# Optimization experiments

Hardware: AMD Instinct MI355X
Metric: run time of the kernel (lower is better)

## Reference

```python
import jax, jax.numpy as jnp
import numpy as np

# dims per module source / chosen globals
B, LB = 4, 28            # new frames, buffered frames; M = B+LB = L = 32
DK, DV = 256, 32         # Dk=256 hardcoded; Dv = 4*len_of_lookup+4 with len_of_lookup=7
HS, WS = 64, 64          # H//8, W//8 with H=W=512
LMAX = 32                # memory cap L
TRAIN_SZ = 1000          # log base train_sz
ALPHA = 0.5              # blend coefficient (original inits 0, which zeroes the branch)
# log(L*h*w + h*w, train_sz) / sqrt(Dk)
SCALE = float(np.log(LMAX * HS * WS + HS * WS) / np.log(TRAIN_SZ) / np.sqrt(DK))


def _xavier(key, fan_in, fan_out):
    lim = np.sqrt(6.0 / (fan_in + fan_out))
    return jax.random.uniform(key, (fan_in, fan_out), jnp.float32, -lim, lim)


def setup_inputs() -> dict:
    key = jax.random.key(0)
    ks = jax.random.split(key, 7)
    return {
        "fc": jax.random.normal(ks[0], (B, DK, HS, WS), jnp.float32),
        "fm": jax.random.normal(ks[1], (B, DV, HS, WS), jnp.float32),
        "key_buffer": jax.random.normal(ks[2], (LB, DK, HS, WS), jnp.float32),
        "value_buffer": jax.random.normal(ks[3], (LB, DV, HS, WS), jnp.float32),
        "Q": _xavier(ks[4], DK, DK),
        "K": _xavier(ks[5], DK, DK),
        "V": _xavier(ks[6], DV, DV),
    }


def reference(fc, fm, key_buffer, value_buffer, Q, K, V):
    # matmul = einsum('ijkl,jm->imkl'): per-pixel channel mixing
    q = jnp.einsum('bdhw,de->behw', fc, Q)                      # [B,Dk,h,w]
    k = jnp.concatenate([jnp.einsum('bdhw,de->behw', fc, K), key_buffer], axis=0)    # [M,Dk,h,w]
    v = jnp.concatenate([jnp.einsum('bdhw,de->behw', fm, V), value_buffer], axis=0)  # [M,Dv,h,w]
    # current_batch (=1) < L, so no slicing of k/v on this step
    scores = SCALE * jnp.einsum('bdhw,mdhw->bmhw', q, k)        # [B,M,h,w]
    attn = jax.nn.softmax(scores, axis=-1)                      # NOTE: softmax over width axis, as in source (dim=-1)
    ctx = jnp.einsum('bmhw,mdhw->bdhw', attn, v)                # [B,Dv,h,w]
    return fm + ALPHA * ctx
```

## Files before the change

### kernel.cpp

```cpp
#include <hip/hip_runtime.h>
#include <hip/hip_bf16.h>
#include <cmath>

#define NB 4
#define NM 32
#define DKc 256
#define DVc 32
#define NP 4096

using bf16x8 = __attribute__((ext_vector_type(8))) short;
using f32x4  = __attribute__((ext_vector_type(4))) float;

__device__ __forceinline__ unsigned short f2bf(float f) {
    union { float f; unsigned u; } x; x.f = f;
    unsigned r = 0x7FFFu + ((x.u >> 16) & 1u);
    return (unsigned short)((x.u + r) >> 16);
}
__device__ __forceinline__ float bflo(unsigned u) { union { unsigned u; float f; } x; x.u = u << 16; return x.f; }
__device__ __forceinline__ float bfhi(unsigned u) { union { unsigned u; float f; } x; x.u = u & 0xffff0000u; return x.f; }
__device__ __forceinline__ float bf2f(unsigned short s) { union { unsigned u; float f; } x; x.u = ((unsigned)s) << 16; return x.f; }

__global__ __launch_bounds__(256) void k_transpose_bf16(
    const float* __restrict__ src, unsigned short* __restrict__ dst,
    int R, int C, long batchStride) {
    __shared__ float tile[64][65];
    int b = blockIdx.z;
    const float* s = src + (long)b * batchStride;
    unsigned short* d = dst + (long)b * batchStride;
    int r0 = blockIdx.y * 64, c0 = blockIdx.x * 64;
    int t = threadIdx.x;
    #pragma unroll
    for (int j = 0; j < 16; ++j) {
        int i = t + 256 * j;
        int r = i >> 6, c = i & 63;
        tile[r][c] = s[(long)(r0 + r) * C + c0 + c];
    }
    __syncthreads();
    #pragma unroll
    for (int j = 0; j < 8; ++j) {
        int i = t + 256 * j;
        int row = i >> 5;
        int pr = i & 31;
        float f0 = tile[2 * pr][row];
        float f1 = tile[2 * pr + 1][row];
        unsigned pack = (unsigned)f2bf(f0) | ((unsigned)f2bf(f1) << 16);
        reinterpret_cast<unsigned*>(d)[(((long)(c0 + row) * R + r0) >> 1) + pr] = pack;
    }
}

__global__ __launch_bounds__(256) void k_vproj(
    const float* __restrict__ fm, const float* __restrict__ V, float* __restrict__ vproj) {
    __shared__ float Vl[32][32];
    __shared__ float fml[32][256];
    int b = blockIdx.y, p0 = blockIdx.x * 256, t = threadIdx.x;
    #pragma unroll
    for (int j = 0; j < 4; ++j) { int i = t + 256 * j; Vl[i >> 5][i & 31] = V[i]; }
    for (int j = 0; j < 32; ++j) {
        int i = t + 256 * j;
        int dd = i >> 8, c = i & 255;
        fml[dd][c] = fm[((long)b * DVc + dd) * NP + p0 + c];
    }
    __syncthreads();
    float acc[32];
    #pragma unroll
    for (int e = 0; e < 32; ++e) acc[e] = 0.f;
    for (int dd = 0; dd < 32; ++dd) {
        float fv = fml[dd][t];
        #pragma unroll
        for (int e = 0; e < 32; ++e) acc[e] += fv * Vl[dd][e];
    }
    #pragma unroll
    for (int e = 0; e < 32; ++e) vproj[((long)b * DVc + e) * NP + p0 + t] = acc[e];
}

__global__ __launch_bounds__(256) void k_proj_gemm(
    const unsigned short* __restrict__ WTq, const unsigned short* __restrict__ WTk,
    const unsigned short* __restrict__ fcT,
    unsigned short* __restrict__ qT, float* __restrict__ kproj) {
    int t = threadIdx.x;
    int wave = t >> 6, lane = t & 63;
    int b = blockIdx.z & 3, mat = blockIdx.z >> 2;
    int e0 = blockIdx.y * 64 + wave * 16;
    int p0 = blockIdx.x * 64;
    int ln = lane & 15, quad = lane >> 4;
    const unsigned short* WT = mat ? WTk : WTq;
    const unsigned short* aptr = WT + (long)(e0 + ln) * DKc + quad * 8;
    const unsigned short* bbase = fcT + ((long)b * NP + p0 + ln) * DKc + quad * 8;
    f32x4 acc[4] = {};
    for (int kk = 0; kk < DKc; kk += 32) {
        bf16x8 a = *reinterpret_cast<const bf16x8*>(aptr + kk);
        #pragma unroll
        for (int j = 0; j < 4; ++j) {
            bf16x8 bb = *reinterpret_cast<const bf16x8*>(bbase + (long)j * 16 * DKc + kk);
            acc[j] = __builtin_amdgcn_mfma_f32_16x16x32_bf16(a, bb, acc[j], 0, 0, 0);
        }
    }
    int eb = e0 + quad * 4;
    if (mat == 0) {
        #pragma unroll
        for (int j = 0; j < 4; ++j)
            #pragma unroll
            for (int r = 0; r < 4; ++r) {
                int e = eb + r, p = p0 + j * 16 + ln;
                qT[((long)b * NP + p) * DKc + e] = f2bf(acc[j][r]);
            }
    } else {
        #pragma unroll
        for (int j = 0; j < 4; ++j)
            #pragma unroll
            for (int r = 0; r < 4; ++r) {
                int e = eb + r, p = p0 + j * 16 + ln;
                kproj[((long)b * DKc + e) * NP + p] = acc[j][r];
            }
    }
}

__global__ __launch_bounds__(512) void k_scores(
    const unsigned short* __restrict__ qT, const float* __restrict__ kproj,
    const float* __restrict__ kbuf, float* __restrict__ scores, float scale) {
    __shared__ float red[16][4][4][32];
    int t = threadIdx.x;
    int g = t >> 5, p = t & 31;
    int p0 = blockIdx.x * 32;
    int mg = blockIdx.y;
    float qreg[4][16];
    #pragma unroll
    for (int b = 0; b < 4; ++b) {
        const uint4* qp4 = reinterpret_cast<const uint4*>(qT + ((long)b * NP + p0 + p) * DKc + g * 16);
        uint4 u0 = qp4[0], u1 = qp4[1];
        unsigned w[8] = {u0.x, u0.y, u0.z, u0.w, u1.x, u1.y, u1.z, u1.w};
        #pragma unroll
        for (int j = 0; j < 8; ++j) { qreg[b][2 * j] = bflo(w[j]); qreg[b][2 * j + 1] = bfhi(w[j]); }
    }
    for (int c = 0; c < 4; ++c) {
        float acc[4][4];
        #pragma unroll
        for (int mi = 0; mi < 4; ++mi)
            #pragma unroll
            for (int b = 0; b < 4; ++b) acc[mi][b] = 0.f;
        #pragma unroll
        for (int mi = 0; mi < 4; ++mi) {
            int m = mg * 16 + c * 4 + mi;
            const float* kp = (m < 4 ? kproj + (long)m * DKc * NP : kbuf + (long)(m - 4) * DKc * NP)
                              + (long)(g * 16) * NP + p0 + p;
            #pragma unroll
            for (int j = 0; j < 16; ++j) {
                float kv = kp[(long)j * NP];
                acc[mi][0] += qreg[0][j] * kv;
                acc[mi][1] += qreg[1][j] * kv;
                acc[mi][2] += qreg[2][j] * kv;
                acc[mi][3] += qreg[3][j] * kv;
            }
        }
        #pragma unroll
        for (int mi = 0; mi < 4; ++mi)
            #pragma unroll
            for (int b = 0; b < 4; ++b) red[g][mi][b][p] = acc[mi][b];
        __syncthreads();
        {
            int mi = t >> 7, b = (t >> 5) & 3, pp = t & 31;
            float s = 0.f;
            #pragma unroll
            for (int gg = 0; gg < 16; ++gg) s += red[gg][mi][b][pp];
            int m = mg * 16 + c * 4 + mi;
            scores[((long)b * NM + m) * NP + p0 + pp] = scale * s;
        }
        __syncthreads();
    }
}

__global__ __launch_bounds__(256) void k_out(
    const float* __restrict__ scores, const float* __restrict__ vproj,
    const float* __restrict__ vbuf, const float* __restrict__ fm,
    float* __restrict__ out) {
    __shared__ unsigned short attn[128][130];
    int t = threadIdx.x;
    int p0 = blockIdx.x * 128;
    int dq = blockIdx.y;
    {
        int b = t >> 6, mrow = (t >> 1) & 31, hs = t & 1;
        const f32x4* s4 = reinterpret_cast<const f32x4*>(scores + ((long)b * NM + mrow) * NP + p0 + hs * 64);
        f32x4 v[16];
        #pragma unroll
        for (int j = 0; j < 16; ++j) v[j] = s4[j];
        float mx = v[0][0];
        #pragma unroll
        for (int j = 0; j < 16; ++j)
            #pragma unroll
            for (int k = 0; k < 4; ++k) mx = fmaxf(mx, v[j][k]);
        float sum = 0.f;
        #pragma unroll
        for (int j = 0; j < 16; ++j)
            #pragma unroll
            for (int k = 0; k < 4; ++k) { float e = __expf(v[j][k] - mx); v[j][k] = e; sum += e; }
        float inv = 1.f / sum;
        unsigned short* arow = &attn[(b << 5) | mrow][hs * 64];
        #pragma unroll
        for (int j = 0; j < 16; ++j)
            #pragma unroll
            for (int k = 0; k < 4; ++k) arow[j * 4 + k] = f2bf(v[j][k] * inv);
    }
    __syncthreads();
    int p = t & 127, grp = t >> 7;
    int b0 = grp * 2, b1 = grp * 2 + 1;
    float acc0[8], acc1[8];
    #pragma unroll
    for (int d = 0; d < 8; ++d) { acc0[d] = 0.f; acc1[d] = 0.f; }
    for (int m = 0; m < 32; ++m) {
        float a0 = bf2f(attn[b0 * 32 + m][p]);
        float a1 = bf2f(attn[b1 * 32 + m][p]);
        const float* vbp = (m < 4 ? vproj + (long)m * DVc * NP : vbuf + (long)(m - 4) * DVc * NP)
                           + (long)(dq * 8) * NP + p0 + p;
        #pragma unroll
        for (int d = 0; d < 8; ++d) {
            float vv = vbp[(long)d * NP];
            acc0[d] += a0 * vv;
            acc1[d] += a1 * vv;
        }
    }
    #pragma unroll
    for (int d = 0; d < 8; ++d) {
        long i0 = ((long)b0 * DVc + dq * 8 + d) * NP + p0 + p;
        out[i0] = fm[i0] + 0.5f * acc0[d];
        long i1 = ((long)b1 * DVc + dq * 8 + d) * NP + p0 + p;
        out[i1] = fm[i1] + 0.5f * acc1[d];
    }
}

extern "C" void kernel_launch(void* const* d_in, const int* in_sizes, int n_in,
                              void* d_out, int out_size, void* d_ws, size_t ws_size,
                              hipStream_t stream) {
    const float* fc = (const float*)d_in[0];
    const float* fm = (const float*)d_in[1];
    const float* kb = (const float*)d_in[2];
    const float* vb = (const float*)d_in[3];
    const float* Q  = (const float*)d_in[4];
    const float* K  = (const float*)d_in[5];
    const float* V  = (const float*)d_in[6];
    float* out = (float*)d_out;
    char* ws = (char*)d_ws;
    unsigned short* fcT   = (unsigned short*)(ws);
    unsigned short* WTq   = (unsigned short*)(ws + 8388608);
    unsigned short* WTk   = (unsigned short*)(ws + 8519680);
    unsigned short* qT    = (unsigned short*)(ws + 8650752);
    float*          kproj = (float*)(ws + 17039360);
    float*          vproj = (float*)(ws + 33816576);
    float*          scores= (float*)(ws + 35913728);
    float scale = (float)(log(135168.0) / log(1000.0) / 16.0);

    hipLaunchKernelGGL(k_transpose_bf16, dim3(64, 4, 4), dim3(256), 0, stream,
                       fc, fcT, 256, 4096, (long)256 * 4096);
    hipLaunchKernelGGL(k_transpose_bf16, dim3(4, 4, 1), dim3(256), 0, stream,
                       Q, WTq, 256, 256, (long)0);
    hipLaunchKernelGGL(k_transpose_bf16, dim3(4, 4, 1), dim3(256), 0, stream,
                       K, WTk, 256, 256, (long)0);
    hipLaunchKernelGGL(k_vproj, dim3(16, 4), dim3(256), 0, stream, fm, V, vproj);
    hipLaunchKernelGGL(k_proj_gemm, dim3(64, 4, 8), dim3(256), 0, stream,
                       WTq, WTk, fcT, qT, kproj);
    hipLaunchKernelGGL(k_scores, dim3(128, 2), dim3(512), 0, stream,
                       qT, kproj, kb, scores, scale);
    hipLaunchKernelGGL(k_out, dim3(32, 4), dim3(256), 0, stream,
                       scores, vproj, vb, fm, out);
}
```

Before: 267.5 us.

## Fuse scores, softmax and output into one kernel; merge prep kernels; widen GEMM tiles

```diff
diff --git a/kernel.cpp b/kernel.cpp
--- a/kernel.cpp
+++ b/kernel.cpp
@@ -16,214 +16,227 @@
     unsigned r = 0x7FFFu + ((x.u >> 16) & 1u);
     return (unsigned short)((x.u + r) >> 16);
 }
-__device__ __forceinline__ float bflo(unsigned u) { union { unsigned u; float f; } x; x.u = u << 16; return x.f; }
-__device__ __forceinline__ float bfhi(unsigned u) { union { unsigned u; float f; } x; x.u = u & 0xffff0000u; return x.f; }
 __device__ __forceinline__ float bf2f(unsigned short s) { union { unsigned u; float f; } x; x.u = ((unsigned)s) << 16; return x.f; }
 
-__global__ __launch_bounds__(256) void k_transpose_bf16(
-    const float* __restrict__ src, unsigned short* __restrict__ dst,
-    int R, int C, long batchStride) {
-    __shared__ float tile[64][65];
-    int b = blockIdx.z;
-    const float* s = src + (long)b * batchStride;
-    unsigned short* d = dst + (long)b * batchStride;
-    int r0 = blockIdx.y * 64, c0 = blockIdx.x * 64;
+__global__ __launch_bounds__(256) void k_prep(
+    const float* __restrict__ fc, unsigned short* __restrict__ fcT,
+    const float* __restrict__ Q, unsigned short* __restrict__ WTq,
+    const float* __restrict__ K, unsigned short* __restrict__ WTk,
+    const float* __restrict__ fm, const float* __restrict__ V, float* __restrict__ vproj) {
+    int x = blockIdx.x;
     int t = threadIdx.x;
-    #pragma unroll
-    for (int j = 0; j < 16; ++j) {
-        int i = t + 256 * j;
-        int r = i >> 6, c = i & 63;
-        tile[r][c] = s[(long)(r0 + r) * C + c0 + c];
-    }
-    __syncthreads();
-    #pragma unroll
-    for (int j = 0; j < 8; ++j) {
-        int i = t + 256 * j;
-        int row = i >> 5;
-        int pr = i & 31;
-        float f0 = tile[2 * pr][row];
-        float f1 = tile[2 * pr + 1][row];
-        unsigned pack = (unsigned)f2bf(f0) | ((unsigned)f2bf(f1) << 16);
-        reinterpret_cast<unsigned*>(d)[(((long)(c0 + row) * R + r0) >> 1) + pr] = pack;
-    }
-}
-
-__global__ __launch_bounds__(256) void k_vproj(
-    const float* __restrict__ fm, const float* __restrict__ V, float* __restrict__ vproj) {
-    __shared__ float Vl[32][32];
-    __shared__ float fml[32][256];
-    int b = blockIdx.y, p0 = blockIdx.x * 256, t = threadIdx.x;
-    #pragma unroll
-    for (int j = 0; j < 4; ++j) { int i = t + 256 * j; Vl[i >> 5][i & 31] = V[i]; }
-    for (int j = 0; j < 32; ++j) {
-        int i = t + 256 * j;
-        int dd = i >> 8, c = i & 255;
-        fml[dd][c] = fm[((long)b * DVc + dd) * NP + p0 + c];
-    }
-    __syncthreads();
-    float acc[32];
-    #pragma unroll
-    for (int e = 0; e < 32; ++e) acc[e] = 0.f;
-    for (int dd = 0; dd < 32; ++dd) {
-        float fv = fml[dd][t];
-        #pragma unroll
-        for (int e = 0; e < 32; ++e) acc[e] += fv * Vl[dd][e];
-    }
-    #pragma unroll
-    for (int e = 0; e < 32; ++e) vproj[((long)b * DVc + e) * NP + p0 + t] = acc[e];
-}
-
-__global__ __launch_bounds__(256) void k_proj_gemm(
+    if (x < 1056) {
+        __shared__ float tile[64][65];
+        const float* s; unsigned short* d; int R, C, r0, c0;
+        if (x < 1024) {
+            int bb = x >> 8, rest = x & 255;
+            R = 256; C = 4096;
+            r0 = (rest >> 6) * 64; c0 = (rest & 63) * 64;
+            s = fc + (long)bb * 256 * 4096; d = fcT + (long)bb * 256 * 4096;
+        } else {
+            int i = x - 1024;
+            int mat = i >> 4, idx = i & 15;
+            R = 256; C = 256;
+            r0 = (idx >> 2) * 64; c0 = (idx & 3) * 64;
+            s = mat ? K : Q; d = mat ? WTk : WTq;
+        }
+        #pragma unroll
+        for (int j = 0; j < 16; ++j) {
+            int i = t + 256 * j;
+            int r = i >> 6, c = i & 63;
+            tile[r][c] = s[(long)(r0 + r) * C + c0 + c];
+        }
+        __syncthreads();
+        #pragma unroll
+        for (int j = 0; j < 8; ++j) {
+            int i = t + 256 * j;
+            int row = i >> 5;
+            int pr = i & 31;
+            float f0 = tile[2 * pr][row];
+            float f1 = tile[2 * pr + 1][row];
+            unsigned pack = (unsigned)f2bf(f0) | ((unsigned)f2bf(f1) << 16);
+            reinterpret_cast<unsigned*>(d)[(((long)(c0 + row) * R + r0) >> 1) + pr] = pack;
+        }
+    } else {
+        __shared__ float Vl[32][32];
+        __shared__ float fml[32][256];
+        int i = x - 1056;
+        int b = i >> 4, p0 = (i & 15) * 256;
+        #pragma unroll
+        for (int j = 0; j < 4; ++j) { int ii = t + 256 * j; Vl[ii >> 5][ii & 31] = V[ii]; }
+        for (int j = 0; j < 32; ++j) {
+            int ii = t + 256 * j;
+            int dd = ii >> 8, c = ii & 255;
+            fml[dd][c] = fm[((long)b * DVc + dd) * NP + p0 + c];
+        }
+        __syncthreads();
+        float acc[32];
+        #pragma unroll
+        for (int e = 0; e < 32; ++e) acc[e] = 0.f;
+        for (int dd = 0; dd < 32; ++dd) {
+            float fv = fml[dd][t];
+            #pragma unroll
+            for (int e = 0; e < 32; ++e) acc[e] += fv * Vl[dd][e];
+        }
+        #pragma unroll
+        for (int e = 0; e < 32; ++e) vproj[((long)b * DVc + e) * NP + p0 + t] = acc[e];
+    }
+}
+
+__global__ __launch_bounds__(256) void k_proj(
     const unsigned short* __restrict__ WTq, const unsigned short* __restrict__ WTk,
     const unsigned short* __restrict__ fcT,
     unsigned short* __restrict__ qT, float* __restrict__ kproj) {
     int t = threadIdx.x;
     int wave = t >> 6, lane = t & 63;
-    int b = blockIdx.z & 3, mat = blockIdx.z >> 2;
-    int e0 = blockIdx.y * 64 + wave * 16;
+    int y = blockIdx.y;
+    int b = y & 3, mat = y >> 2;
     int p0 = blockIdx.x * 64;
     int ln = lane & 15, quad = lane >> 4;
     const unsigned short* WT = mat ? WTk : WTq;
-    const unsigned short* aptr = WT + (long)(e0 + ln) * DKc + quad * 8;
+    int e0w = wave * 64;
     const unsigned short* bbase = fcT + ((long)b * NP + p0 + ln) * DKc + quad * 8;
-    f32x4 acc[4] = {};
+    f32x4 acc[4][4] = {};
     for (int kk = 0; kk < DKc; kk += 32) {
-        bf16x8 a = *reinterpret_cast<const bf16x8*>(aptr + kk);
-        #pragma unroll
-        for (int j = 0; j < 4; ++j) {
-            bf16x8 bb = *reinterpret_cast<const bf16x8*>(bbase + (long)j * 16 * DKc + kk);
-            acc[j] = __builtin_amdgcn_mfma_f32_16x16x32_bf16(a, bb, acc[j], 0, 0, 0);
-        }
-    }
-    int eb = e0 + quad * 4;
+        bf16x8 a[4], bb[4];
+        #pragma unroll
+        for (int i = 0; i < 4; ++i)
+            a[i] = *reinterpret_cast<const bf16x8*>(WT + (long)(e0w + i * 16 + ln) * DKc + quad * 8 + kk);
+        #pragma unroll
+        for (int j = 0; j < 4; ++j)
+            bb[j] = *reinterpret_cast<const bf16x8*>(bbase + (long)j * 16 * DKc + kk);
+        #pragma unroll
+        for (int i = 0; i < 4; ++i)
+            #pragma unroll
+            for (int j = 0; j < 4; ++j)
+                acc[i][j] = __builtin_amdgcn_mfma_f32_16x16x32_bf16(a[i], bb[j], acc[i][j], 0, 0, 0);
+    }
     if (mat == 0) {
         #pragma unroll
-        for (int j = 0; j < 4; ++j)
-            #pragma unroll
-            for (int r = 0; r < 4; ++r) {
-                int e = eb + r, p = p0 + j * 16 + ln;
-                qT[((long)b * NP + p) * DKc + e] = f2bf(acc[j][r]);
-            }
+        for (int i = 0; i < 4; ++i)
+            #pragma unroll
+            for (int j = 0; j < 4; ++j)
+                #pragma unroll
+                for (int r = 0; r < 4; ++r) {
+                    int e = e0w + i * 16 + quad * 4 + r, p = p0 + j * 16 + ln;
+                    qT[((long)b * NP + p) * DKc + e] = f2bf(acc[i][j][r]);
+                }
     } else {
         #pragma unroll
-        for (int j = 0; j < 4; ++j)
-            #pragma unroll
-            for (int r = 0; r < 4; ++r) {
-                int e = eb + r, p = p0 + j * 16 + ln;
-                kproj[((long)b * DKc + e) * NP + p] = acc[j][r];
-            }
-    }
-}
-
-__global__ __launch_bounds__(512) void k_scores(
+        for (int i = 0; i < 4; ++i)
+            #pragma unroll
+            for (int j = 0; j < 4; ++j)
+                #pragma unroll
+                for (int r = 0; r < 4; ++r) {
+                    int e = e0w + i * 16 + quad * 4 + r, p = p0 + j * 16 + ln;
+                    kproj[((long)b * DKc + e) * NP + p] = acc[i][j][r];
+                }
+    }
+}
+
+__global__ __launch_bounds__(512, 2) void k_fused(
     const unsigned short* __restrict__ qT, const float* __restrict__ kproj,
-    const float* __restrict__ kbuf, float* __restrict__ scores, float scale) {
-    __shared__ float red[16][4][4][32];
+    const float* __restrict__ kbuf, const float* __restrict__ vproj,
+    const float* __restrict__ vbuf, const float* __restrict__ fm,
+    float* __restrict__ out, float scale) {
+    __shared__ float smemf[256 * 68];
+    __shared__ float sc[32][68];
+    float (*LDSq)[68] = reinterpret_cast<float (*)[68]>(smemf);
+    float (*red)[32][68] = reinterpret_cast<float (*)[32][68]>(smemf);
     int t = threadIdx.x;
-    int g = t >> 5, p = t & 31;
-    int p0 = blockIdx.x * 32;
-    int mg = blockIdx.y;
-    float qreg[4][16];
-    #pragma unroll
-    for (int b = 0; b < 4; ++b) {
-        const uint4* qp4 = reinterpret_cast<const uint4*>(qT + ((long)b * NP + p0 + p) * DKc + g * 16);
-        uint4 u0 = qp4[0], u1 = qp4[1];
-        unsigned w[8] = {u0.x, u0.y, u0.z, u0.w, u1.x, u1.y, u1.z, u1.w};
-        #pragma unroll
-        for (int j = 0; j < 8; ++j) { qreg[b][2 * j] = bflo(w[j]); qreg[b][2 * j + 1] = bfhi(w[j]); }
-    }
-    for (int c = 0; c < 4; ++c) {
-        float acc[4][4];
-        #pragma unroll
-        for (int mi = 0; mi < 4; ++mi)
-            #pragma unroll
-            for (int b = 0; b < 4; ++b) acc[mi][b] = 0.f;
-        #pragma unroll
-        for (int mi = 0; mi < 4; ++mi) {
-            int m = mg * 16 + c * 4 + mi;
-            const float* kp = (m < 4 ? kproj + (long)m * DKc * NP : kbuf + (long)(m - 4) * DKc * NP)
-                              + (long)(g * 16) * NP + p0 + p;
-            #pragma unroll
-            for (int j = 0; j < 16; ++j) {
-                float kv = kp[(long)j * NP];
-                acc[mi][0] += qreg[0][j] * kv;
-                acc[mi][1] += qreg[1][j] * kv;
-                acc[mi][2] += qreg[2][j] * kv;
-                acc[mi][3] += qreg[3][j] * kv;
-            }
-        }
-        #pragma unroll
-        for (int mi = 0; mi < 4; ++mi)
-            #pragma unroll
-            for (int b = 0; b < 4; ++b) red[g][mi][b][p] = acc[mi][b];
-        __syncthreads();
-        {
-            int mi = t >> 7, b = (t >> 5) & 3, pp = t & 31;
-            float s = 0.f;
-            #pragma unroll
-            for (int gg = 0; gg < 16; ++gg) s += red[gg][mi][b][pp];
-            int m = mg * 16 + c * 4 + mi;
-            scores[((long)b * NM + m) * NP + p0 + pp] = scale * s;
-        }
-        __syncthreads();
-    }
-}
-
-__global__ __launch_bounds__(256) void k_out(
-    const float* __restrict__ scores, const float* __restrict__ vproj,
-    const float* __restrict__ vbuf, const float* __restrict__ fm,
-    float* __restrict__ out) {
-    __shared__ unsigned short attn[128][130];
-    int t = threadIdx.x;
-    int p0 = blockIdx.x * 128;
-    int dq = blockIdx.y;
-    {
-        int b = t >> 6, mrow = (t >> 1) & 31, hs = t & 1;
-        const f32x4* s4 = reinterpret_cast<const f32x4*>(scores + ((long)b * NM + mrow) * NP + p0 + hs * 64);
-        f32x4 v[16];
-        #pragma unroll
-        for (int j = 0; j < 16; ++j) v[j] = s4[j];
-        float mx = v[0][0];
-        #pragma unroll
-        for (int j = 0; j < 16; ++j)
-            #pragma unroll
-            for (int k = 0; k < 4; ++k) mx = fmaxf(mx, v[j][k]);
-        float sum = 0.f;
-        #pragma unroll
-        for (int j = 0; j < 16; ++j)
-            #pragma unroll
-            for (int k = 0; k < 4; ++k) { float e = __expf(v[j][k] - mx); v[j][k] = e; sum += e; }
-        float inv = 1.f / sum;
-        unsigned short* arow = &attn[(b << 5) | mrow][hs * 64];
-        #pragma unroll
-        for (int j = 0; j < 16; ++j)
-            #pragma unroll
-            for (int k = 0; k < 4; ++k) arow[j * 4 + k] = f2bf(v[j][k] * inv);
-    }
-    __syncthreads();
-    int p = t & 127, grp = t >> 7;
-    int b0 = grp * 2, b1 = grp * 2 + 1;
-    float acc0[8], acc1[8];
-    #pragma unroll
-    for (int d = 0; d < 8; ++d) { acc0[d] = 0.f; acc1[d] = 0.f; }
-    for (int m = 0; m < 32; ++m) {
-        float a0 = bf2f(attn[b0 * 32 + m][p]);
-        float a1 = bf2f(attn[b1 * 32 + m][p]);
-        const float* vbp = (m < 4 ? vproj + (long)m * DVc * NP : vbuf + (long)(m - 4) * DVc * NP)
-                           + (long)(dq * 8) * NP + p0 + p;
-        #pragma unroll
-        for (int d = 0; d < 8; ++d) {
-            float vv = vbp[(long)d * NP];
-            acc0[d] += a0 * vv;
-            acc1[d] += a1 * vv;
-        }
-    }
-    #pragma unroll
-    for (int d = 0; d < 8; ++d) {
-        long i0 = ((long)b0 * DVc + dq * 8 + d) * NP + p0 + p;
-        out[i0] = fm[i0] + 0.5f * acc0[d];
-        long i1 = ((long)b1 * DVc + dq * 8 + d) * NP + p0 + p;
-        out[i1] = fm[i1] + 0.5f * acc1[d];
+    int b = blockIdx.x >> 6, hrow = blockIdx.x & 63;
+    int p0h = hrow * 64;
+
+    {
+        const unsigned short* qtile = qT + ((long)b * NP + p0h) * DKc;
+        int ec = t >> 6, p = t & 63;
+        #pragma unroll
+        for (int s = 0; s < 4; ++s) {
+            int e0 = ec * 32 + s * 8;
+            bf16x8 v8 = *reinterpret_cast<const bf16x8*>(qtile + (long)p * DKc + e0);
+            #pragma unroll
+            for (int i = 0; i < 8; ++i) LDSq[e0 + i][p] = bf2f((unsigned short)v8[i]);
+        }
+    }
+    __syncthreads();
+
+    int wq = t & 15, eg = t >> 4;
+    f32x4 q4[8];
+    #pragma unroll
+    for (int j = 0; j < 8; ++j)
+        q4[j] = *reinterpret_cast<const f32x4*>(&LDSq[eg * 8 + j][wq * 4]);
+    __syncthreads();
+
+    f32x4 acc[NM];
+    #pragma unroll
+    for (int m = 0; m < NM; ++m) acc[m] = (f32x4){0.f, 0.f, 0.f, 0.f};
+    #pragma unroll
+    for (int m = 0; m < NM; ++m) {
+        const float* kp = (m < 4 ? kproj + (long)m * DKc * NP : kbuf + (long)(m - 4) * DKc * NP)
+                          + (long)(eg * 8) * NP + p0h + wq * 4;
+        #pragma unroll
+        for (int j = 0; j < 8; ++j) {
+            f32x4 kv = *reinterpret_cast<const f32x4*>(kp + (long)j * NP);
+            acc[m] += q4[j] * kv;
+        }
+    }
+    #pragma unroll
+    for (int m = 0; m < NM; ++m)
+        #pragma unroll
+        for (int c = 0; c < 4; ++c) {
+            float v = acc[m][c];
+            v += __shfl_xor(v, 16);
+            v += __shfl_xor(v, 32);
+            acc[m][c] = v;
+        }
+    int wave = t >> 6, lane = t & 63;
+    if (lane < 16) {
+        #pragma unroll
+        for (int m = 0; m < NM; ++m)
+            *reinterpret_cast<f32x4*>(&red[wave][m][lane * 4]) = acc[m];
+    }
+    __syncthreads();
+    {
+        int m = t >> 4, w0 = (t & 15) * 4;
+        f32x4 s = (f32x4){0.f, 0.f, 0.f, 0.f};
+        #pragma unroll
+        for (int v = 0; v < 8; ++v) s += *reinterpret_cast<const f32x4*>(&red[v][m][w0]);
+        f32x4 sv = s * scale;
+        *reinterpret_cast<f32x4*>(&sc[m][w0]) = sv;
+    }
+    __syncthreads();
+    {
+        #pragma unroll
+        for (int r = 0; r < 4; ++r) {
+            int m = wave * 4 + r;
+            float x = sc[m][lane];
+            float mx = x;
+            #pragma unroll
+            for (int d = 1; d < 64; d <<= 1) mx = fmaxf(mx, __shfl_xor(mx, d));
+            float e = __expf(x - mx);
+            float sum = e;
+            #pragma unroll
+            for (int d = 1; d < 64; d <<= 1) sum += __shfl_xor(sum, d);
+            sc[m][lane] = e / sum;
+        }
+    }
+    __syncthreads();
+    {
+        int w = t & 63, dg = t >> 6;
+        f32x4 c = (f32x4){0.f, 0.f, 0.f, 0.f};
+        #pragma unroll
+        for (int m = 0; m < NM; ++m) {
+            float a = sc[m][w];
+            const float* vp = (m < 4 ? vproj + (long)m * DVc * NP : vbuf + (long)(m - 4) * DVc * NP)
+                              + (long)(dg * 4) * NP + p0h + w;
+            #pragma unroll
+            for (int i = 0; i < 4; ++i) c[i] += a * vp[(long)i * NP];
+        }
+        #pragma unroll
+        for (int i = 0; i < 4; ++i) {
+            long gi = ((long)b * DVc + dg * 4 + i) * NP + p0h + w;
+            out[gi] = fm[gi] + 0.5f * c[i];
+        }
     }
 }
 
@@ -245,20 +258,12 @@
     unsigned short* qT    = (unsigned short*)(ws + 8650752);
     float*          kproj = (float*)(ws + 17039360);
     float*          vproj = (float*)(ws + 33816576);
-    float*          scores= (float*)(ws + 35913728);
     float scale = (float)(log(135168.0) / log(1000.0) / 16.0);
 
-    hipLaunchKernelGGL(k_transpose_bf16, dim3(64, 4, 4), dim3(256), 0, stream,
-                       fc, fcT, 256, 4096, (long)256 * 4096);
-    hipLaunchKernelGGL(k_transpose_bf16, dim3(4, 4, 1), dim3(256), 0, stream,
-                       Q, WTq, 256, 256, (long)0);
-    hipLaunchKernelGGL(k_transpose_bf16, dim3(4, 4, 1), dim3(256), 0, stream,
-                       K, WTk, 256, 256, (long)0);
-    hipLaunchKernelGGL(k_vproj, dim3(16, 4), dim3(256), 0, stream, fm, V, vproj);
-    hipLaunchKernelGGL(k_proj_gemm, dim3(64, 4, 8), dim3(256), 0, stream,
+    hipLaunchKernelGGL(k_prep, dim3(1120), dim3(256), 0, stream,
+                       fc, fcT, Q, WTq, K, WTk, fm, V, vproj);
+    hipLaunchKernelGGL(k_proj, dim3(64, 8), dim3(256), 0, stream,
                        WTq, WTk, fcT, qT, kproj);
-    hipLaunchKernelGGL(k_scores, dim3(128, 2), dim3(512), 0, stream,
-                       qT, kproj, kb, scores, scale);
-    hipLaunchKernelGGL(k_out, dim3(32, 4), dim3(256), 0, stream,
-                       scores, vproj, vb, fm, out);
-}
+    hipLaunchKernelGGL(k_fused, dim3(256), dim3(512), 0, stream,
+                       qT, kproj, kb, vproj, vb, fm, out, scale);
+}
```

Result: faster. 257.0 us (-3.9%).
